# Performance work log

Measured on AMD Instinct MI355X. Metric: run time of the kernel, lower is better.

## Reference

```python
import jax, jax.numpy as jnp
import numpy as np

N, E, IN, H, OUT, L, G = 50000, 800000, 128, 128, 64, 3, 64
NEG_SLOPE = 0.2


def setup_inputs() -> dict:
    key = jax.random.key(0)
    ks = jax.random.split(key, 10)
    x = jax.random.normal(ks[0], (N, IN), dtype=jnp.float32)
    edge_index = jax.random.randint(ks[1], (2, E), 0, N, dtype=jnp.int64)
    batch = jnp.sort(jax.random.randint(ks[2], (N,), 0, G, dtype=jnp.int64))
    s_in = 1.0 / np.sqrt(IN)
    s_h = 1.0 / np.sqrt(H)
    return {
        "x": x,
        "edge_index": edge_index,
        "batch": batch,
        "W0": jax.random.normal(ks[3], (IN, H), dtype=jnp.float32) * s_in,
        "b0": jnp.zeros((H,), dtype=jnp.float32),
        "Wl": jax.random.normal(ks[4], (L, H, H), dtype=jnp.float32) * s_h,
        "a_src": jax.random.normal(ks[5], (L, H), dtype=jnp.float32) * s_h,
        "a_dst": jax.random.normal(ks[6], (L, H), dtype=jnp.float32) * s_h,
        "bl": jnp.zeros((L, H), dtype=jnp.float32),
        "Wf": jax.random.normal(ks[7], (H, OUT), dtype=jnp.float32) * s_h,
        "bf": jnp.zeros((OUT,), dtype=jnp.float32),
    }


def _gat_layer(h, src, dst, n_nodes, W, a_s, a_d, b):
    # GATConv, heads=1: h' = W h; e_ij = leaky_relu(a_s.h'_j + a_d.h'_i)
    hp = h @ W  # [N, H]
    alpha_s = hp @ a_s  # [N]
    alpha_d = hp @ a_d  # [N]
    e = jax.nn.leaky_relu(alpha_s[src] + alpha_d[dst], NEG_SLOPE)  # [E+N]
    # segment softmax over incoming edges of each destination node
    m = jax.ops.segment_max(e, dst, num_segments=n_nodes)
    ex = jnp.exp(e - m[dst])
    denom = jax.ops.segment_sum(ex, dst, num_segments=n_nodes)
    alpha = ex / denom[dst]  # [E+N]
    out = jax.ops.segment_sum(hp[src] * alpha[:, None], dst, num_segments=n_nodes)
    return out + b


def reference(x, edge_index, batch, W0, b0, Wl, a_src, a_dst, bl, Wf, bf):
    n_nodes = x.shape[0]
    loops = jnp.arange(n_nodes, dtype=edge_index.dtype)
    src = jnp.concatenate([edge_index[0], loops])  # add_self_loops=True
    dst = jnp.concatenate([edge_index[1], loops])
    h = x @ W0 + b0  # initial Linear
    n_layers = Wl.shape[0]
    for l in range(n_layers):
        h = _gat_layer(h, src, dst, n_nodes, Wl[l], a_src[l], a_dst[l], bl[l])
        if l < n_layers - 1:
            h = jax.nn.relu(h)  # BasicGNN: act between layers, none after last
    pooled = jax.ops.segment_sum(h, batch, num_segments=G)  # global_add_pool
    return (pooled @ Wf + bf).squeeze()
```

## Files before the change

### kernel.cpp

```cpp
#include <hip/hip_runtime.h>
#include <hip/hip_bf16.h>
#include <math.h>

#define HF 128
#define GCOUNT 64
#define OUTF 64
#define NEG 0.2f
#define CH 2048
#define BCAP 8192

typedef unsigned short u16;
typedef unsigned int   u32;
typedef unsigned char  u8;
typedef short bf16x8 __attribute__((ext_vector_type(8)));
typedef float f32x4  __attribute__((ext_vector_type(4)));
typedef float f32x2  __attribute__((ext_vector_type(2)));

__device__ __forceinline__ u16 f2b(float f) {
    u32 u = __builtin_bit_cast(u32, f);
    u32 r = (u + 0x7FFFu + ((u >> 16) & 1u)) >> 16;
    return (u16)r;
}

__device__ __forceinline__ u8 f2q(float f) {
    return (u8)(__builtin_amdgcn_cvt_pk_fp8_f32(f, f, 0, false) & 0xFF);
}

__global__ void k_pack_init(const float* __restrict__ W0, const float* __restrict__ Wl,
                            u16* __restrict__ P, int* bucketCur, float* pooled) {
    if (blockIdx.x < 32) {
        int m = blockIdx.x >> 3;
        int i = (blockIdx.x & 7) * 256 + threadIdx.x;
        const float* W = (m == 0) ? W0 : Wl + (size_t)(m - 1) * HF * HF;
        u16* Pm = P + (size_t)m * HF * HF;
        int lane = i & 63, kc = (i >> 6) & 3, t = i >> 8;
        int quad = lane >> 4, col = 16 * t + (lane & 15);
        #pragma unroll
        for (int j = 0; j < 8; ++j) {
            int k = kc * 32 + quad * 8 + j;
            Pm[(size_t)i * 8 + j] = f2b(W[k * HF + col]);
        }
    } else if (blockIdx.x == 32) {
        bucketCur[threadIdx.x] = threadIdx.x * BCAP;
    } else {
        pooled[(blockIdx.x - 33) * 256 + threadIdx.x] = 0.f;
    }
}

__device__ __forceinline__ void dev_bpart(int bx, const int* __restrict__ esrc,
                                          const int* __restrict__ edst,
                                          int* __restrict__ bucketCur,
                                          u32* __restrict__ epart, int ne, int ntot) {
    __shared__ int cnt[256];
    __shared__ int base[256];
    int tid = threadIdx.x;
    int t0 = bx * CH, t1 = min(t0 + CH, ntot);
    cnt[tid] = 0;
    __syncthreads();
    int sreg[8], dreg[8];
    #pragma unroll
    for (int it = 0; it < 8; ++it) {
        int t = t0 + tid + it * 256;
        int s = 0, d = -1;
        if (t < t1) {
            if (t < ne) { s = esrc[t]; d = edst[t]; }
            else        { s = t - ne; d = s; }
            atomicAdd(&cnt[d >> 8], 1);
        }
        sreg[it] = s; dreg[it] = d;
    }
    __syncthreads();
    int c = cnt[tid];
    base[tid] = c ? atomicAdd(&bucketCur[tid], c) : 0;
    cnt[tid] = 0;
    __syncthreads();
    #pragma unroll
    for (int it = 0; it < 8; ++it) {
        int d = dreg[it];
        if (d >= 0) {
            int b = d >> 8;
            int pos = base[b] + atomicAdd(&cnt[b], 1);
            epart[pos] = ((u32)sreg[it] << 8) | (u32)(d & 255);
        }
    }
}

__device__ __forceinline__ void dev_bcsr(int bx, const u32* __restrict__ epart,
                                         const int* __restrict__ bucketCur,
                                         int* __restrict__ rowbeg,
                                         int* __restrict__ rowend,
                                         int* __restrict__ colidx, int n) {
    __shared__ int deg[256], offs[256], curs[256], s[256];
    int b = bx, tid = threadIdx.x;
    int e0 = b * BCAP, e1 = bucketCur[b];
    deg[tid] = 0;
    curs[tid] = 0;
    __syncthreads();
    for (int t = e0 + tid; t < e1; t += 256)
        atomicAdd(&deg[epart[t] & 255u], 1);
    __syncthreads();
    int v = deg[tid];
    s[tid] = v;
    __syncthreads();
    int acc = v;
    for (int off = 1; off < 256; off <<= 1) {
        int t = (tid >= off) ? s[tid - off] : 0;
        __syncthreads();
        acc += t;
        s[tid] = acc;
        __syncthreads();
    }
    int excl = acc - v;
    offs[tid] = excl;
    int node = (b << 8) + tid;
    if (node < n) {
        rowbeg[node] = e0 + excl;
        rowend[node] = e0 + excl + v;
    }
    __syncthreads();
    for (int t = e0 + tid; t < e1; t += 256) {
        u32 e = epart[t];
        int l = e & 255u;
        int pos = e0 + offs[l] + atomicAdd(&curs[l], 1);
        colidx[pos] = (int)(e >> 8);
    }
}

template<bool A32, bool Q8>
__device__ __forceinline__ void dev_gemm(int bx, const u16* __restrict__ Ab,
                                         const float* __restrict__ Af,
                                         const u16* __restrict__ Bp,
                                         const float* __restrict__ bias,
                                         const float* __restrict__ a_s,
                                         const float* __restrict__ a_d,
                                         float* __restrict__ as_,
                                         float* __restrict__ ad_,
                                         u16* __restrict__ C,
                                         u8* __restrict__ C8, int M) {
    int lane = threadIdx.x & 63;
    int wave = threadIdx.x >> 6;
    int quad = lane >> 4, l16 = lane & 15;
    int m0 = bx * 64 + wave * 16;
    int arow = m0 + l16;
    bool aval = arow < M;
    const bf16x8* Av = A32 ? nullptr : (const bf16x8*)(Ab + (size_t)arow * HF);
    const bf16x8* Bv = (const bf16x8*)Bp;
    f32x4 acc[8] = {};

    #pragma unroll
    for (int kc = 0; kc < 4; ++kc) {
        bf16x8 a = {};
        if (aval) {
            if constexpr (A32) {
                const float* ap = Af + (size_t)arow * HF + kc * 32 + quad * 8;
                float4 f0 = *(const float4*)ap;
                float4 f1 = *(const float4*)(ap + 4);
                a[0] = (short)f2b(f0.x); a[1] = (short)f2b(f0.y);
                a[2] = (short)f2b(f0.z); a[3] = (short)f2b(f0.w);
                a[4] = (short)f2b(f1.x); a[5] = (short)f2b(f1.y);
                a[6] = (short)f2b(f1.z); a[7] = (short)f2b(f1.w);
            } else {
                a = Av[kc * 4 + quad];
            }
        }
        #pragma unroll
        for (int t = 0; t < 8; ++t)
            acc[t] = __builtin_amdgcn_mfma_f32_16x16x32_bf16(a, Bv[t * 256 + kc * 64 + lane],
                                                             acc[t], 0, 0, 0);
    }

    int orow0 = m0 + quad * 4;
    #pragma unroll
    for (int t = 0; t < 8; ++t) {
        float b4 = bias ? bias[t * 16 + l16] : 0.f;
        #pragma unroll
        for (int r = 0; r < 4; ++r) {
            int orow = orow0 + r;
            if (orow < M) {
                float v = acc[t][r] + b4;
                if constexpr (Q8) C8[(size_t)orow * HF + t * 16 + l16] = f2q(v);
                else              C [(size_t)orow * HF + t * 16 + l16] = f2b(v);
            }
        }
    }

    if (as_) {
        float avs[8], avd[8];
        #pragma unroll
        for (int t = 0; t < 8; ++t) {
            avs[t] = a_s[t * 16 + l16];
            avd[t] = a_d[t * 16 + l16];
        }
        #pragma unroll
        for (int r = 0; r < 4; ++r) {
            float ps = 0.f, pd = 0.f;
            #pragma unroll
            for (int t = 0; t < 8; ++t) {
                ps = fmaf(acc[t][r], avs[t], ps);
                pd = fmaf(acc[t][r], avd[t], pd);
            }
            #pragma unroll
            for (int o = 1; o < 16; o <<= 1) {
                ps += __shfl_xor(ps, o);
                pd += __shfl_xor(pd, o);
            }
            int row = orow0 + r;
            if (l16 == 0 && row < M) { as_[row] = ps; ad_[row] = pd; }
        }
    }
}

__global__ __launch_bounds__(256) void k_gemm0_bpart(const float* __restrict__ x,
                                                     const u16* __restrict__ Wp,
                                                     const float* __restrict__ b0,
                                                     u16* __restrict__ hb, int M, int gemmb,
                                                     const int* __restrict__ esrc,
                                                     const int* __restrict__ edst,
                                                     int* __restrict__ bucketCur,
                                                     u32* __restrict__ epart, int ne, int ntot) {
    if ((int)blockIdx.x < gemmb)
        dev_gemm<true, false>(blockIdx.x, nullptr, x, Wp, b0,
                              nullptr, nullptr, nullptr, nullptr, hb, nullptr, M);
    else
        dev_bpart(blockIdx.x - gemmb, esrc, edst, bucketCur, epart, ne, ntot);
}

__global__ __launch_bounds__(256) void k_gemm1_bcsr(const u16* __restrict__ hb,
                                                    const u16* __restrict__ Bp,
                                                    const float* __restrict__ a_s,
                                                    const float* __restrict__ a_d,
                                                    float* __restrict__ as_,
                                                    float* __restrict__ ad_,
                                                    u8* __restrict__ hp8, int M, int gemmb,
                                                    const u32* __restrict__ epart,
                                                    const int* __restrict__ bucketCur,
                                                    int* __restrict__ rowbeg,
                                                    int* __restrict__ rowend,
                                                    int* __restrict__ colidx, int n) {
    if ((int)blockIdx.x < gemmb)
        dev_gemm<false, true>(blockIdx.x, hb, nullptr, Bp, nullptr,
                              a_s, a_d, as_, ad_, nullptr, hp8, M);
    else
        dev_bcsr(blockIdx.x - gemmb, epart, bucketCur, rowbeg, rowend, colidx, n);
}

__global__ __launch_bounds__(256) void k_gemm_layer(const u16* __restrict__ hb,
                                                    const u16* __restrict__ Bp,
                                                    const float* __restrict__ a_s,
                                                    const float* __restrict__ a_d,
                                                    float* __restrict__ as_,
                                                    float* __restrict__ ad_,
                                                    u8* __restrict__ hp8, int M) {
    dev_gemm<false, true>(blockIdx.x, hb, nullptr, Bp, nullptr,
                          a_s, a_d, as_, ad_, nullptr, hp8, M);
}

template<bool POOL>
__device__ __forceinline__ void dev_agg_item(int it, const int* __restrict__ rowbeg,
                                             const int* __restrict__ rowend,
                                             const int* __restrict__ colidx,
                                             const u8* __restrict__ hp8,
                                             const float* __restrict__ as_,
                                             const float* __restrict__ ad_,
                                             const float* __restrict__ bl,
                                             u16* __restrict__ hout,
                                             int n, int relu,
                                             const int* __restrict__ batch,
                                             float* __restrict__ pooled) {
    int wv = threadIdx.x >> 6;
    int node = it * 4 + wv;
    int lane = threadIdx.x & 63;
    bool valid = node < n;
    int beg = 0, end = 0;
    float adi = 0.f;
    if (valid) { beg = rowbeg[node]; end = rowend[node]; adi = ad_[node]; }
    int deg = end - beg;
    int cnt = deg < 64 ? deg : 64;
    int npair = (cnt + 1) >> 1;

    int srcl = (lane < deg) ? colidx[beg + lane] : 0;

    int hl = lane & 31;
    int half = lane >> 5;

    u32 q[8];
    int pf = npair < 8 ? npair : 8;
    #pragma unroll
    for (int i = 0; i < 8; ++i) {
        int e  = 2 * i + half;
        int ec = e < cnt ? e : (cnt > 0 ? cnt - 1 : 0);
        int s  = __shfl(srcl, ec);
        if (i < pf) q[i] = ((const u32*)(hp8 + (size_t)s * HF))[hl];
    }

    float el = 0.f;
    if (lane < deg) {
        float e = as_[srcl] + adi;
        e = e > 0.f ? e : NEG * e;
        el = __expf(e);
    }
    float ssum = el;
    for (int jj = beg + 64 + lane; jj < end; jj += 64) {
        float e = as_[colidx[jj]] + adi;
        e = e > 0.f ? e : NEG * e;
        ssum += __expf(e);
    }
    #pragma unroll
    for (int off = 32; off; off >>= 1) ssum += __shfl_xor(ssum, off);
    float wl = el;

    float a0 = 0.f, a1 = 0.f, a2 = 0.f, a3 = 0.f;
    #pragma unroll
    for (int i = 0; i < 8; ++i) {
        int e  = 2 * i + half;
        int ec = e < cnt ? e : (cnt > 0 ? cnt - 1 : 0);
        float w = (e < cnt) ? __shfl(wl, ec) : 0.f;
        if (i < pf) {
            u32 v = q[i];
            f32x2 lo = __builtin_amdgcn_cvt_pk_f32_fp8((int)v, false);
            f32x2 hi = __builtin_amdgcn_cvt_pk_f32_fp8((int)v, true);
            a0 = fmaf(w, lo.x, a0); a1 = fmaf(w, lo.y, a1);
            a2 = fmaf(w, hi.x, a2); a3 = fmaf(w, hi.y, a3);
        }
    }
    for (int p = 8; p < npair; ++p) {
        int e  = 2 * p + half;
        int ec = e < cnt ? e : cnt - 1;
        int   s = __shfl(srcl, ec);
        float w = (e < cnt) ? __shfl(wl, ec) : 0.f;
        u32 v = ((const u32*)(hp8 + (size_t)s * HF))[hl];
        f32x2 lo = __builtin_amdgcn_cvt_pk_f32_fp8((int)v, false);
        f32x2 hi = __builtin_amdgcn_cvt_pk_f32_fp8((int)v, true);
        a0 = fmaf(w, lo.x, a0); a1 = fmaf(w, lo.y, a1);
        a2 = fmaf(w, hi.x, a2); a3 = fmaf(w, hi.y, a3);
    }
    for (int jj = beg + 64; jj < end; ++jj) {
        int srcn = colidx[jj];
        float e = as_[srcn] + adi;
        e = e > 0.f ? e : NEG * e;
        float w = (half == 0) ? __expf(e) : 0.f;
        u32 v = ((const u32*)(hp8 + (size_t)srcn * HF))[hl];
        f32x2 lo = __builtin_amdgcn_cvt_pk_f32_fp8((int)v, false);
        f32x2 hi = __builtin_amdgcn_cvt_pk_f32_fp8((int)v, true);
        a0 = fmaf(w, lo.x, a0); a1 = fmaf(w, lo.y, a1);
        a2 = fmaf(w, hi.x, a2); a3 = fmaf(w, hi.y, a3);
    }

    a0 += __shfl_xor(a0, 32); a1 += __shfl_xor(a1, 32);
    a2 += __shfl_xor(a2, 32); a3 += __shfl_xor(a3, 32);

    if constexpr (!POOL) {
        if (half == 0 && valid) {
            float inv = 1.f / ssum;
            float4 bb = ((const float4*)bl)[hl];
            a0 = fmaf(a0, inv, bb.x); a1 = fmaf(a1, inv, bb.y);
            a2 = fmaf(a2, inv, bb.z); a3 = fmaf(a3, inv, bb.w);
            if (relu) {
                a0 = fmaxf(a0, 0.f); a1 = fmaxf(a1, 0.f);
                a2 = fmaxf(a2, 0.f); a3 = fmaxf(a3, 0.f);
            }
            uint2 o;
            o.x = ((u32)f2b(a1) << 16) | (u32)f2b(a0);
            o.y = ((u32)f2b(a3) << 16) | (u32)f2b(a2);
            ((uint2*)(hout + (size_t)node * HF))[hl] = o;
        }
    } else {
        __shared__ float ptile[4][HF];
        if (half == 0) {
            float o0 = 0.f, o1 = 0.f, o2 = 0.f, o3 = 0.f;
            if (valid) {
                float inv = 1.f / ssum;
                float4 bb = ((const float4*)bl)[hl];
                o0 = fmaf(a0, inv, bb.x); o1 = fmaf(a1, inv, bb.y);
                o2 = fmaf(a2, inv, bb.z); o3 = fmaf(a3, inv, bb.w);
            }
            ptile[wv][hl * 4 + 0] = o0; ptile[wv][hl * 4 + 1] = o1;
            ptile[wv][hl * 4 + 2] = o2; ptile[wv][hl * 4 + 3] = o3;
        }
        __syncthreads();
        int tid = threadIdx.x;
        if (tid < HF) {
            float a = 0.f;
            int curb = -1;
            #pragma unroll
            for (int s2 = 0; s2 < 4; ++s2) {
                int nd = it * 4 + s2;
                if (nd < n) {
                    int b = batch[nd];
                    if (b != curb) {
                        if (curb >= 0) atomicAdd(&pooled[curb * HF + tid], a);
                        curb = b;
                        a = 0.f;
                    }
                    a += ptile[s2][tid];
                }
            }
            if (curb >= 0) atomicAdd(&pooled[curb * HF + tid], a);
        }
    }
}

__global__ __launch_bounds__(256) void k_agg(const int* __restrict__ rowbeg,
                                             const int* __restrict__ rowend,
                                             const int* __restrict__ colidx,
                                             const u8* __restrict__ hp8,
                                             const float* __restrict__ as_,
                                             const float* __restrict__ ad_,
                                             const float* __restrict__ bl,
                                             u16* __restrict__ hout,
                                             int n, int relu) {
    dev_agg_item<false>(blockIdx.x, rowbeg, rowend, colidx, hp8, as_, ad_, bl,
                        hout, n, relu, nullptr, nullptr);
}

__global__ __launch_bounds__(256) void k_agg_pool(const int* __restrict__ rowbeg,
                                                  const int* __restrict__ rowend,
                                                  const int* __restrict__ colidx,
                                                  const u8* __restrict__ hp8,
                                                  const float* __restrict__ as_,
                                                  const float* __restrict__ ad_,
                                                  const float* __restrict__ bl,
                                                  int n,
                                                  const int* __restrict__ batch,
                                                  float* __restrict__ pooled) {
    dev_agg_item<true>(blockIdx.x, rowbeg, rowend, colidx, hp8, as_, ad_, bl,
                       nullptr, n, 0, batch, pooled);
}

__global__ void k_final(const float* __restrict__ pooled, const float* __restrict__ Wf,
                        const float* __restrict__ bf, float* __restrict__ out) {
    int g = blockIdx.x, o = threadIdx.x;
    float acc = bf[o];
    #pragma unroll 8
    for (int k = 0; k < HF; ++k) acc = fmaf(pooled[g * HF + k], Wf[k * OUTF + o], acc);
    out[g * OUTF + o] = acc;
}

extern "C" void kernel_launch(void* const* d_in, const int* in_sizes, int n_in,
                              void* d_out, int out_size, void* d_ws, size_t ws_size,
                              hipStream_t stream) {
    const float* x      = (const float*)d_in[0];
    const int*   edge   = (const int*)d_in[1];
    const int*   batch  = (const int*)d_in[2];
    const float* W0     = (const float*)d_in[3];
    const float* b0     = (const float*)d_in[4];
    const float* Wl     = (const float*)d_in[5];
    const float* a_src  = (const float*)d_in[6];
    const float* a_dst  = (const float*)d_in[7];
    const float* bl     = (const float*)d_in[8];
    const float* Wf     = (const float*)d_in[9];
    const float* bf     = (const float*)d_in[10];
    float* out = (float*)d_out;

    const int N  = in_sizes[2];
    const int E  = in_sizes[1] / 2;
    const int Et = E + N;
    const int L  = 3;
    const int NB = (N + 255) >> 8;

    char* ws = (char*)d_ws;
    size_t off = 0;
    auto alloc = [&](size_t bytes) { char* p = ws + off; off += (bytes + 255) & ~(size_t)255; return p; };
    u16*   hb      = (u16*)alloc((size_t)N * HF * 2);
    u8*    hp8     = (u8*)alloc((size_t)N * HF);
    u16*   Wp      = (u16*)alloc((size_t)4 * HF * HF * 2);
    float* as_     = (float*)alloc((size_t)N * 4);
    float* ad_     = (float*)alloc((size_t)N * 4);
    int*   rowbeg  = (int*)alloc((size_t)N * 4);
    int*   rowend  = (int*)alloc((size_t)N * 4);
    int*   colidx  = (int*)alloc((size_t)NB * BCAP * 4);
    u32*   epart   = (u32*)alloc((size_t)NB * BCAP * 4);
    int*   bucketCur = (int*)alloc(256 * 4);
    float* pooled  = (float*)alloc((size_t)GCOUNT * HF * 4);
    (void)ws_size; (void)n_in; (void)out_size;

    const int wb4   = (N + 3) / 4;
    const int gemmb = (N + 63) / 64;
    const int partb = (Et + CH - 1) / CH;

    const int* esrc = edge;
    const int* edst = edge + E;

    k_pack_init<<<65, 256, 0, stream>>>(W0, Wl, Wp, bucketCur, pooled);

    k_gemm0_bpart<<<gemmb + partb, 256, 0, stream>>>(x, Wp, b0, hb, N, gemmb,
                                                     esrc, edst, bucketCur, epart, E, Et);

    k_gemm1_bcsr<<<gemmb + NB, 256, 0, stream>>>(hb, Wp + (size_t)1 * HF * HF,
                                                 a_src, a_dst, as_, ad_, hp8, N, gemmb,
                                                 epart, bucketCur, rowbeg, rowend, colidx, N);

    for (int l = 0; l < L; ++l) {
        if (l > 0)
            k_gemm_layer<<<gemmb, 256, 0, stream>>>(hb, Wp + (size_t)(l + 1) * HF * HF,
                                                    a_src + l * HF, a_dst + l * HF,
                                                    as_, ad_, hp8, N);
        if (l < L - 1)
            k_agg<<<wb4, 256, 0, stream>>>(rowbeg, rowend, colidx, hp8, as_, ad_,
                                           bl + l * HF, hb, N, 1);
        else
            k_agg_pool<<<wb4, 256, 0, stream>>>(rowbeg, rowend, colidx, hp8, as_, ad_,
                                                bl + l * HF, N, batch, pooled);
    }

    k_final<<<GCOUNT, OUTF, 0, stream>>>(pooled, Wf, bf, out);
}
```

Measured before the change: 261.0 us.

## Assign one node per half-wave in GAT aggregation instead of one per wave

The aggregation kernel now maps each 32-lane half-wave to its own destination node, so each block handles 8 nodes instead of 4. This drops the cross-half reduction and the pair-interleaved edge split, and uses 32-wide shuffles. Prefetch depth grows to 16 edges, with batched 8-edge loads for edges 16 to 31. With an average degree around 17, this should raise useful lanes per wave and memory-level parallelism. In exchange, each node's edges are processed serially by fewer lanes and register pressure is higher.

```diff
diff --git a/kernel.cpp b/kernel.cpp
--- a/kernel.cpp
+++ b/kernel.cpp
@@ -255,6 +255,14 @@
                           a_s, a_d, as_, ad_, nullptr, hp8, M);
 }
 
+__device__ __forceinline__ void agg_fma4(u32 v, float w,
+                                         float& a0, float& a1, float& a2, float& a3) {
+    f32x2 lo = __builtin_amdgcn_cvt_pk_f32_fp8((int)v, false);
+    f32x2 hi = __builtin_amdgcn_cvt_pk_f32_fp8((int)v, true);
+    a0 = fmaf(w, lo.x, a0); a1 = fmaf(w, lo.y, a1);
+    a2 = fmaf(w, hi.x, a2); a3 = fmaf(w, hi.y, a3);
+}
+
 template<bool POOL>
 __device__ __forceinline__ void dev_agg_item(int it, const int* __restrict__ rowbeg,
                                              const int* __restrict__ rowend,
@@ -268,89 +276,80 @@
                                              const int* __restrict__ batch,
                                              float* __restrict__ pooled) {
     int wv = threadIdx.x >> 6;
-    int node = it * 4 + wv;
     int lane = threadIdx.x & 63;
+    int half = lane >> 5;
+    int hl = lane & 31;
+    int slot = wv * 2 + half;
+    int node = it * 8 + slot;
     bool valid = node < n;
     int beg = 0, end = 0;
     float adi = 0.f;
     if (valid) { beg = rowbeg[node]; end = rowend[node]; adi = ad_[node]; }
     int deg = end - beg;
-    int cnt = deg < 64 ? deg : 64;
-    int npair = (cnt + 1) >> 1;
-
-    int srcl = (lane < deg) ? colidx[beg + lane] : 0;
-
-    int hl = lane & 31;
-    int half = lane >> 5;
-
-    u32 q[8];
-    int pf = npair < 8 ? npair : 8;
-    #pragma unroll
-    for (int i = 0; i < 8; ++i) {
-        int e  = 2 * i + half;
-        int ec = e < cnt ? e : (cnt > 0 ? cnt - 1 : 0);
-        int s  = __shfl(srcl, ec);
+    int cnt = deg < 32 ? deg : 32;
+    int ecmax = cnt > 1 ? cnt - 1 : 0;
+
+    int srcl = (hl < deg) ? colidx[beg + hl] : 0;
+
+    u32 q[16];
+    int pf = cnt < 16 ? cnt : 16;
+    #pragma unroll
+    for (int i = 0; i < 16; ++i) {
+        int ec = i < cnt ? i : ecmax;
+        int s = __shfl(srcl, ec, 32);
         if (i < pf) q[i] = ((const u32*)(hp8 + (size_t)s * HF))[hl];
     }
 
     float el = 0.f;
-    if (lane < deg) {
+    if (hl < deg) {
         float e = as_[srcl] + adi;
         e = e > 0.f ? e : NEG * e;
         el = __expf(e);
     }
     float ssum = el;
-    for (int jj = beg + 64 + lane; jj < end; jj += 64) {
+    for (int jj = beg + 32 + hl; jj < end; jj += 32) {
         float e = as_[colidx[jj]] + adi;
         e = e > 0.f ? e : NEG * e;
         ssum += __expf(e);
     }
     #pragma unroll
-    for (int off = 32; off; off >>= 1) ssum += __shfl_xor(ssum, off);
+    for (int off = 16; off; off >>= 1) ssum += __shfl_xor(ssum, off, 32);
     float wl = el;
 
     float a0 = 0.f, a1 = 0.f, a2 = 0.f, a3 = 0.f;
     #pragma unroll
-    for (int i = 0; i < 8; ++i) {
-        int e  = 2 * i + half;
-        int ec = e < cnt ? e : (cnt > 0 ? cnt - 1 : 0);
-        float w = (e < cnt) ? __shfl(wl, ec) : 0.f;
-        if (i < pf) {
-            u32 v = q[i];
-            f32x2 lo = __builtin_amdgcn_cvt_pk_f32_fp8((int)v, false);
-            f32x2 hi = __builtin_amdgcn_cvt_pk_f32_fp8((int)v, true);
-            a0 = fmaf(w, lo.x, a0); a1 = fmaf(w, lo.y, a1);
-            a2 = fmaf(w, hi.x, a2); a3 = fmaf(w, hi.y, a3);
-        }
-    }
-    for (int p = 8; p < npair; ++p) {
-        int e  = 2 * p + half;
-        int ec = e < cnt ? e : cnt - 1;
-        int   s = __shfl(srcl, ec);
-        float w = (e < cnt) ? __shfl(wl, ec) : 0.f;
+    for (int i = 0; i < 16; ++i) {
+        float w = (i < cnt) ? __shfl(wl, i, 32) : 0.f;
+        if (i < pf) agg_fma4(q[i], w, a0, a1, a2, a3);
+    }
+    for (int base = 16; base < cnt; base += 8) {
+        u32 r[8];
+        int mrem = cnt - base < 8 ? cnt - base : 8;
+        #pragma unroll
+        for (int i = 0; i < 8; ++i) {
+            int ec = base + i < cnt ? base + i : ecmax;
+            int s = __shfl(srcl, ec, 32);
+            if (i < mrem) r[i] = ((const u32*)(hp8 + (size_t)s * HF))[hl];
+        }
+        #pragma unroll
+        for (int i = 0; i < 8; ++i) {
+            if (i < mrem) {
+                float w = __shfl(wl, base + i, 32);
+                agg_fma4(r[i], w, a0, a1, a2, a3);
+            }
+        }
+    }
+    for (int jj = beg + 32; jj < end; ++jj) {
+        int s = colidx[jj];
+        float e = as_[s] + adi;
+        e = e > 0.f ? e : NEG * e;
+        float w = __expf(e);
         u32 v = ((const u32*)(hp8 + (size_t)s * HF))[hl];
-        f32x2 lo = __builtin_amdgcn_cvt_pk_f32_fp8((int)v, false);
-        f32x2 hi = __builtin_amdgcn_cvt_pk_f32_fp8((int)v, true);
-        a0 = fmaf(w, lo.x, a0); a1 = fmaf(w, lo.y, a1);
-        a2 = fmaf(w, hi.x, a2); a3 = fmaf(w, hi.y, a3);
-    }
-    for (int jj = beg + 64; jj < end; ++jj) {
-        int srcn = colidx[jj];
-        float e = as_[srcn] + adi;
-        e = e > 0.f ? e : NEG * e;
-        float w = (half == 0) ? __expf(e) : 0.f;
-        u32 v = ((const u32*)(hp8 + (size_t)srcn * HF))[hl];
-        f32x2 lo = __builtin_amdgcn_cvt_pk_f32_fp8((int)v, false);
-        f32x2 hi = __builtin_amdgcn_cvt_pk_f32_fp8((int)v, true);
-        a0 = fmaf(w, lo.x, a0); a1 = fmaf(w, lo.y, a1);
-        a2 = fmaf(w, hi.x, a2); a3 = fmaf(w, hi.y, a3);
-    }
-
-    a0 += __shfl_xor(a0, 32); a1 += __shfl_xor(a1, 32);
-    a2 += __shfl_xor(a2, 32); a3 += __shfl_xor(a3, 32);
+        agg_fma4(v, w, a0, a1, a2, a3);
+    }
 
     if constexpr (!POOL) {
-        if (half == 0 && valid) {
+        if (valid) {
             float inv = 1.f / ssum;
             float4 bb = ((const float4*)bl)[hl];
             a0 = fmaf(a0, inv, bb.x); a1 = fmaf(a1, inv, bb.y);
@@ -365,17 +364,14 @@
             ((uint2*)(hout + (size_t)node * HF))[hl] = o;
         }
     } else {
-        __shared__ float ptile[4][HF];
-        if (half == 0) {
-            float o0 = 0.f, o1 = 0.f, o2 = 0.f, o3 = 0.f;
-            if (valid) {
-                float inv = 1.f / ssum;
-                float4 bb = ((const float4*)bl)[hl];
-                o0 = fmaf(a0, inv, bb.x); o1 = fmaf(a1, inv, bb.y);
-                o2 = fmaf(a2, inv, bb.z); o3 = fmaf(a3, inv, bb.w);
-            }
-            ptile[wv][hl * 4 + 0] = o0; ptile[wv][hl * 4 + 1] = o1;
-            ptile[wv][hl * 4 + 2] = o2; ptile[wv][hl * 4 + 3] = o3;
+        __shared__ float ptile[8][HF];
+        {
+            float inv = valid ? 1.f / ssum : 0.f;
+            float4 bb = ((const float4*)bl)[hl];
+            ptile[slot][hl * 4 + 0] = valid ? fmaf(a0, inv, bb.x) : 0.f;
+            ptile[slot][hl * 4 + 1] = valid ? fmaf(a1, inv, bb.y) : 0.f;
+            ptile[slot][hl * 4 + 2] = valid ? fmaf(a2, inv, bb.z) : 0.f;
+            ptile[slot][hl * 4 + 3] = valid ? fmaf(a3, inv, bb.w) : 0.f;
         }
         __syncthreads();
         int tid = threadIdx.x;
@@ -383,8 +379,8 @@
             float a = 0.f;
             int curb = -1;
             #pragma unroll
-            for (int s2 = 0; s2 < 4; ++s2) {
-                int nd = it * 4 + s2;
+            for (int s2 = 0; s2 < 8; ++s2) {
+                int nd = it * 8 + s2;
                 if (nd < n) {
                     int b = batch[nd];
                     if (b != curb) {
@@ -474,7 +470,7 @@
     float* pooled  = (float*)alloc((size_t)GCOUNT * HF * 4);
     (void)ws_size; (void)n_in; (void)out_size;
 
-    const int wb4   = (N + 3) / 4;
+    const int wb8   = (N + 7) / 8;
     const int gemmb = (N + 63) / 64;
     const int partb = (Et + CH - 1) / CH;
 
@@ -496,10 +492,10 @@
                                                     a_src + l * HF, a_dst + l * HF,
                                                     as_, ad_, hp8, N);
         if (l < L - 1)
-            k_agg<<<wb4, 256, 0, stream>>>(rowbeg, rowend, colidx, hp8, as_, ad_,
+            k_agg<<<wb8, 256, 0, stream>>>(rowbeg, rowend, colidx, hp8, as_, ad_,
                                            bl + l * HF, hb, N, 1);
         else
-            k_agg_pool<<<wb4, 256, 0, stream>>>(rowbeg, rowend, colidx, hp8, as_, ad_,
+            k_agg_pool<<<wb8, 256, 0, stream>>>(rowbeg, rowend, colidx, hp8, as_, ad_,
                                                 bl + l * HF, N, batch, pooled);
     }
 
```

Result: faster. 236.3 us (-9.5%).
